# Performance work log

Hardware: AMD Instinct MI355X
Metric: run time of the kernel (lower is better)

Reference implementation:

```python
import jax, jax.numpy as jnp
import numpy as np

B, S, D, HW = 256, 32, 512, 196


def setup_inputs() -> dict:
    key = jax.random.key(0)
    ks = jax.random.split(key, 34)
    n = lambda k, sh, s=1.0: jax.random.normal(k, sh, dtype=jnp.float32) * s
    w = 0.03  # xavier-ish scale for D=512 layers
    return {
        "words": n(ks[0], (B, S, D)),
        "question": n(ks[1], (B, 2 * D)),
        "know": n(ks[2], (B, D, HW)),
        "control0": n(ks[3], (B, D)),
        "memory0": n(ks[4], (B, D)),
        # ControlUnit
        "Wsc": n(ks[5], (2 * D, D), w), "bsc": jnp.zeros((D,), jnp.float32),
        "Wp": n(ks[6], (D, D), w), "bp": jnp.zeros((D,), jnp.float32),
        "Wcq": n(ks[7], (2 * D, D), w), "bcq": jnp.zeros((D,), jnp.float32),
        "wac": n(ks[8], (D, 1), w), "bac": jnp.zeros((1,), jnp.float32),
        # ReadUnit
        "Wm": n(ks[9], (D, D), w), "bm": jnp.zeros((D,), jnp.float32),
        "Wk": n(ks[10], (D, D), w), "bk": jnp.zeros((D,), jnp.float32),
        "Wc1": n(ks[11], (3 * D, D), w), "bc1": jnp.zeros((D,), jnp.float32),
        "Wc2": n(ks[12], (D, D), w), "bc2": jnp.zeros((D,), jnp.float32),
        "war": n(ks[13], (D, 1), w), "bar": jnp.zeros((1,), jnp.float32),
        # WriteUnit (self-attention variant)
        "Wwc": n(ks[14], (D, D), w), "bwc": jnp.zeros((D,), jnp.float32),
        "waw": n(ks[15], (D, 1), w), "baw": jnp.zeros((1,), jnp.float32),
        "Wwcat": n(ks[16], (3 * D, D), w), "bwcat": jnp.zeros((D,), jnp.float32),
    }


def reference(words, question, know, control0, memory0,
              Wsc, bsc, Wp, bp, Wcq, bcq, wac, bac,
              Wm, bm, Wk, bk, Wc1, bc1, Wc2, bc2, war, bar,
              Wwc, bwc, waw, baw, Wwcat, bwcat):
    # ---- ControlUnit (step 0) ----
    q = jnp.tanh(question @ Wsc + bsc)                    # [B,D]
    pa = q @ Wp + bp                                      # position_aware[0]
    cq = jnp.concatenate([control0, pa], axis=1) @ Wcq + bcq  # [B,D]
    logit_c = (cq[:, None, :] * words) @ wac + bac        # [B,S,1]
    attn_c = jax.nn.softmax(logit_c, axis=1)
    control = jnp.sum(attn_c * words, axis=1)             # [B,D]

    # ---- ReadUnit ----
    pm = memory0 @ Wm + bm                                # [B,D]
    pk = jnp.einsum('bdn,de->ben', know, Wk) + bk[None, :, None]  # [B,D,HW]
    pm_b = jnp.broadcast_to(pm[:, :, None], pk.shape)
    feat = jnp.concatenate([pm_b * pk, pk, pm_b], axis=1)  # [B,3D,HW]
    h = jax.nn.relu(jnp.einsum('bfn,fd->bnd', feat, Wc1) + bc1)  # [B,HW,D]
    h = h @ Wc2 + bc2                                     # [B,HW,D]
    logit_r = (h * control[:, None, :]) @ war + bar       # [B,HW,1]
    a_r = jax.nn.softmax(logit_r[..., 0], axis=1)          # [B,HW]
    read = jnp.einsum('bdn,bn->bd', know, a_r)            # [B,D]

    # ---- WriteUnit (self-attention over previous controls; T=1 at step 0) ----
    sc = control @ Wwc + bwc                              # [B,D]
    ctrl_prev = control0[:, :, None]                      # [B,D,T]
    logit_w = jnp.einsum('bdt,d->bt', sc[:, :, None] * ctrl_prev, waw[:, 0]) + baw  # [B,T]
    a_w = jax.nn.softmax(logit_w, axis=1)
    attn_mem = jnp.einsum('bdt,bt->bd', memory0[:, :, None], a_w)  # [B,D]
    concat = jnp.concatenate([read, memory0, attn_mem], axis=1)    # [B,3D]
    next_mem = concat @ Wwcat + bwcat                     # [B,D]

    return control, next_mem
```

## Files before the change

### kernel.cpp

```cpp
#include <hip/hip_runtime.h>
#include <hip/hip_bf16.h>
#include <math.h>

typedef __hip_bfloat16 bf16;
typedef __attribute__((ext_vector_type(8))) short s8v;
typedef __attribute__((ext_vector_type(4))) short s4v;
typedef __attribute__((ext_vector_type(4))) float f4v;

#define BB 256
#define SS 32
#define DD 512
#define HWN 196
#define APW 72

__device__ __forceinline__ float b2f(bf16 x){ return __bfloat162float(x); }
__device__ __forceinline__ bf16 f2b(float x){ return __float2bfloat16(x); }
__device__ __forceinline__ float us2f(unsigned short u){
    union { unsigned int i; float f; } t; t.i = ((unsigned int)u) << 16; return t.f;
}
__device__ __forceinline__ float ldin(int dt, const void* p, size_t i){
    return dt ? b2f(((const bf16*)p)[i]) : ((const float*)p)[i];
}

__global__ void detect_k(const void* q, int* flag){
    __shared__ int cnt;
    if (threadIdx.x == 0) cnt = 0;
    __syncthreads();
    const unsigned short* u = (const unsigned short*)q;
    unsigned short v = u[threadIdx.x * 4];
    int e = (v >> 7) & 0xFF;
    atomicAdd(&cnt, (e >= 100 && e <= 140) ? 1 : 0);
    __syncthreads();
    if (threadIdx.x == 0) *flag = (cnt > 128) ? 1 : 0;
}

struct PJob { const void* s; const void* s_b; const void* s2; const void* s2_b;
              bf16* d; int R, C, ldd, kofs, mode, boff; };
struct PrepP { PJob j[11]; const void* war; const void* bk; float* warf; float* bkf; };

__global__ __launch_bounds__(256) void prep_k(PrepP P, const int* __restrict__ flag){
    const int dt = *flag;
    __shared__ float T[32][33];
    int bx = blockIdx.x;
    int ji = 0;
    #pragma unroll
    for (int i = 0; i < 11; ++i) if (bx >= P.j[i].boff) ji = i;
    PJob jb = P.j[ji];
    const void* src  = dt ? jb.s_b  : jb.s;
    const void* src2 = dt ? jb.s2_b : jb.s2;
    int t = bx - jb.boff;
    int tx = threadIdx.x & 31, ty = threadIdx.x >> 5;
    if (jb.mode == 3){
        for (int i = threadIdx.x; i < DD; i += 256){
            P.warf[i] = ldin(dt, P.war, i);
            P.bkf[i]  = ldin(dt, P.bk, i);
        }
        return;
    }
    int nrt = jb.R >> 5;
    int r0 = (t % nrt) << 5, c0 = (t / nrt) << 5;
    if (jb.mode == 2){
        for (int rr = ty; rr < 32; rr += 8)
            jb.d[(size_t)(r0 + rr) * jb.ldd + jb.kofs + c0 + tx] =
                f2b(ldin(dt, src, (size_t)(r0 + rr) * jb.C + c0 + tx));
        return;
    }
    for (int rr = ty; rr < 32; rr += 8){
        float v = ldin(dt, src, (size_t)(r0 + rr) * jb.C + c0 + tx);
        if (jb.mode == 1) v += ldin(dt, src2, (size_t)(r0 + rr) * jb.C + c0 + tx);
        T[rr][tx] = v;
    }
    __syncthreads();
    for (int rr = ty; rr < 32; rr += 8)
        jb.d[(size_t)(c0 + rr) * jb.ldd + jb.kofs + r0 + tx] = f2b(T[tx][rr]);
}

__global__ __launch_bounds__(256) void g1_mfma(const void* __restrict__ know,
                                               const bf16* __restrict__ BT,
                                               const float* __restrict__ bkf,
                                               bf16* __restrict__ C,
                                               int b0, int swz,
                                               const int* __restrict__ flag){
    const int dt = *flag;
    __shared__ __align__(16) bf16 As[128 * APW];
    __shared__ __align__(16) bf16 Bs[128 * APW];
    const int tid = threadIdx.x, lane = tid & 63, wave = tid >> 6;
    const int q = lane >> 4, mr = lane & 15;
    int idb = blockIdx.x, rt, ct;
    if (swz){ int g = idb >> 5, w = idb & 31; rt = g * 8 + (w & 7); ct = w >> 3; }
    else    { rt = idb >> 2; ct = idb & 3; }
    const int r0 = rt * 128, c0 = ct * 128;
    const int quad = tid >> 3;
    const int kg   = tid & 7;
    const int m    = r0 + quad * 4;
    const int bl   = m / HWN;
    const int n    = m - bl * HWN;
    const size_t abase = ((size_t)(b0 + bl) * DD) * HWN + n;
    f4v acc[2][8];
    #pragma unroll
    for (int t = 0; t < 2; ++t)
        #pragma unroll
        for (int j = 0; j < 8; ++j){ f4v z = {0.f,0.f,0.f,0.f}; acc[t][j] = z; }
    for (int k0 = 0; k0 < DD; k0 += 64){
        #pragma unroll
        for (int h = 0; h < 2; ++h){
            int kb = k0 + h * 32 + kg * 4;
            union { bf16 hh[4]; s4v v; } pk_[4];
            if (dt == 0){
                const float* kp = (const float*)know + abase + (size_t)kb * HWN;
                float4 ra  = *(const float4*)kp;
                float4 rb  = *(const float4*)(kp + HWN);
                float4 rc  = *(const float4*)(kp + 2 * HWN);
                float4 rd4 = *(const float4*)(kp + 3 * HWN);
                #pragma unroll
                for (int j = 0; j < 4; ++j){
                    pk_[j].hh[0] = f2b((&ra.x)[j]);
                    pk_[j].hh[1] = f2b((&rb.x)[j]);
                    pk_[j].hh[2] = f2b((&rc.x)[j]);
                    pk_[j].hh[3] = f2b((&rd4.x)[j]);
                }
            } else {
                const unsigned short* kp = (const unsigned short*)know + abase + (size_t)kb * HWN;
                ushort4 ua = *(const ushort4*)kp;
                ushort4 ub = *(const ushort4*)(kp + HWN);
                ushort4 uc = *(const ushort4*)(kp + 2 * HWN);
                ushort4 ud = *(const ushort4*)(kp + 3 * HWN);
                #pragma unroll
                for (int j = 0; j < 4; ++j){
                    ((unsigned short*)&pk_[j].v)[0] = (&ua.x)[j];
                    ((unsigned short*)&pk_[j].v)[1] = (&ub.x)[j];
                    ((unsigned short*)&pk_[j].v)[2] = (&uc.x)[j];
                    ((unsigned short*)&pk_[j].v)[3] = (&ud.x)[j];
                }
            }
            #pragma unroll
            for (int j = 0; j < 4; ++j)
                *(s4v*)&As[(quad * 4 + j) * APW + h * 32 + kg * 4] = pk_[j].v;
        }
        {
            int col = tid >> 1, kb = (tid & 1) * 32;
            const bf16* wp = BT + (size_t)(c0 + col) * DD + k0 + kb;
            bf16* dst = &Bs[col * APW + kb];
            #pragma unroll
            for (int t4 = 0; t4 < 32; t4 += 8)
                *(float4*)(dst + t4) = *(const float4*)(wp + t4);
        }
        __syncthreads();
        #pragma unroll
        for (int h = 0; h < 2; ++h){
            s8v a0 = *(const s8v*)&As[(wave * 32 + mr) * APW + h * 32 + q * 8];
            s8v a1 = *(const s8v*)&As[(wave * 32 + 16 + mr) * APW + h * 32 + q * 8];
            #pragma unroll
            for (int j = 0; j < 8; ++j){
                s8v b = *(const s8v*)&Bs[(j * 16 + mr) * APW + h * 32 + q * 8];
                acc[0][j] = __builtin_amdgcn_mfma_f32_16x16x32_bf16(a0, b, acc[0][j], 0, 0, 0);
                acc[1][j] = __builtin_amdgcn_mfma_f32_16x16x32_bf16(a1, b, acc[1][j], 0, 0, 0);
            }
        }
        __syncthreads();
    }
    #pragma unroll
    for (int t = 0; t < 2; ++t)
        #pragma unroll
        for (int j = 0; j < 8; ++j){
            float bb = bkf[c0 + j * 16 + mr];
            #pragma unroll
            for (int i = 0; i < 4; ++i){
                int row = r0 + wave * 32 + t * 16 + q * 4 + i;
                int col = c0 + j * 16 + mr;
                C[(size_t)row * DD + col] = f2b(acc[t][j][i] + bb);
            }
        }
}

__global__ __launch_bounds__(256) void g2_mfma(const bf16* __restrict__ Apk,
                                               const bf16* __restrict__ BT,
                                               const float* __restrict__ pmf,
                                               const float* __restrict__ t3b,
                                               const float* __restrict__ uf,
                                               float* __restrict__ lpart,
                                               int b0, int swz){
    __shared__ __align__(16) bf16 As[128 * APW];
    __shared__ __align__(16) bf16 Bs[128 * APW];
    const int tid = threadIdx.x, lane = tid & 63, wave = tid >> 6;
    const int q = lane >> 4, mr = lane & 15;
    int idb = blockIdx.x, u, ct;
    if (swz){ int g = idb >> 5, w = idb & 31; u = g * 8 + (w & 7); ct = w >> 3; }
    else    { u = idb >> 2; ct = idb & 3; }
    const int bl = u >> 1, rt = u & 1;
    const int b = b0 + bl;
    const int c0 = ct * 128, rbase = rt * 128;
    const float* pmb = pmf + (size_t)b * DD;
    f4v acc[2][8];
    #pragma unroll
    for (int t = 0; t < 2; ++t)
        #pragma unroll
        for (int j = 0; j < 8; ++j){ f4v z = {0.f,0.f,0.f,0.f}; acc[t][j] = z; }
    for (int k0 = 0; k0 < DD; k0 += 64){
        {
            int row = tid >> 1, kb = (tid & 1) * 32;
            int rl = rbase + row;
            bf16* dst = &As[row * APW + kb];
            if (rl < HWN){
                const bf16* ap = Apk + ((size_t)bl * HWN + rl) * DD + k0 + kb;
                #pragma unroll
                for (int t4 = 0; t4 < 32; t4 += 8)
                    *(float4*)(dst + t4) = *(const float4*)(ap + t4);
            } else {
                float4 z = {0.f,0.f,0.f,0.f};
                #pragma unroll
                for (int t4 = 0; t4 < 32; t4 += 8)
                    *(float4*)(dst + t4) = z;
            }
        }
        {
            int col = tid >> 1, kb = (tid & 1) * 32;
            const bf16* wrow = BT + (size_t)(c0 + col) * (2 * DD) + k0 + kb;
            bf16* dst = &Bs[col * APW + kb];
            #pragma unroll
            for (int t4 = 0; t4 < 32; t4 += 8){
                union { bf16 h[8]; float4 f; } w1, w2, be;
                w1.f = *(const float4*)(wrow + t4);
                w2.f = *(const float4*)(wrow + DD + t4);
                float4 pA = *(const float4*)(pmb + k0 + kb + t4);
                float4 pB = *(const float4*)(pmb + k0 + kb + t4 + 4);
                #pragma unroll
                for (int j = 0; j < 4; ++j){
                    be.h[j]     = f2b((&pA.x)[j] * b2f(w1.h[j])     + b2f(w2.h[j]));
                    be.h[4 + j] = f2b((&pB.x)[j] * b2f(w1.h[4 + j]) + b2f(w2.h[4 + j]));
                }
                *(float4*)(dst + t4) = be.f;
            }
        }
        __syncthreads();
        #pragma unroll
        for (int h = 0; h < 2; ++h){
            s8v a0 = *(const s8v*)&As[(wave * 32 + mr) * APW + h * 32 + q * 8];
            s8v a1 = *(const s8v*)&As[(wave * 32 + 16 + mr) * APW + h * 32 + q * 8];
            #pragma unroll
            for (int j = 0; j < 8; ++j){
                s8v b2 = *(const s8v*)&Bs[(j * 16 + mr) * APW + h * 32 + q * 8];
                acc[0][j] = __builtin_amdgcn_mfma_f32_16x16x32_bf16(a0, b2, acc[0][j], 0, 0, 0);
                acc[1][j] = __builtin_amdgcn_mfma_f32_16x16x32_bf16(a1, b2, acc[1][j], 0, 0, 0);
            }
        }
        __syncthreads();
    }
    float part[2][4] = {};
    #pragma unroll
    for (int t = 0; t < 2; ++t)
        #pragma unroll
        for (int j = 0; j < 8; ++j)
            #pragma unroll
            for (int i = 0; i < 4; ++i){
                int rl = rbase + wave * 32 + t * 16 + q * 4 + i;
                if (rl < HWN){
                    int col = c0 + j * 16 + mr;
                    float hv = acc[t][j][i] + t3b[(size_t)b * DD + col];
                    part[t][i] += fmaxf(hv, 0.f) * uf[(size_t)b * DD + col];
                }
            }
    #pragma unroll
    for (int t = 0; t < 2; ++t)
        #pragma unroll
        for (int i = 0; i < 4; ++i){
            float v = part[t][i];
            v += __shfl_xor(v, 1, 16);
            v += __shfl_xor(v, 2, 16);
            v += __shfl_xor(v, 4, 16);
            v += __shfl_xor(v, 8, 16);
            int rl = rbase + wave * 32 + t * 16 + q * 4 + i;
            if (mr == 0 && rl < HWN)
                lpart[(size_t)ct * (BB * HWN) + (size_t)b * HWN + rl] = v;
        }
}

struct SSeg { const void* A; int a_ws, lda, K, koff; };
struct SP {
    SSeg s[2]; int nseg;
    const bf16* BT; int ldb;
    const float* amul;
    const void* bias;
    float* C; int M, N, act;
    void* out2; int o2off;
};
struct SPP { SP j[2]; };

__global__ __launch_bounds__(256) void sgemm_k(SPP P, const int* __restrict__ flag){
    const int dt = *flag;
    const SP p = P.j[blockIdx.z];
    const int tid = threadIdx.x, lane = tid & 63, w = tid >> 6;
    const int q = lane >> 4, mr = lane & 15;
    const int n0 = blockIdx.x * 16, m0 = blockIdx.y * 64 + w * 16;
    f4v acc = {0.f,0.f,0.f,0.f};
    for (int sg = 0; sg < p.nseg; ++sg){
        const SSeg s = p.s[sg];
        const float* amul = (sg == 0) ? p.amul : nullptr;
        #pragma unroll 4
        for (int k0 = 0; k0 < s.K; k0 += 32){
            const int kk = k0 + q * 8;
            union { bf16 h[8]; s8v v; } a;
            if (s.a_ws || dt == 0){
                const float* Af = (const float*)s.A + (size_t)(m0 + mr) * s.lda + kk;
                float4 f0 = *(const float4*)Af;
                float4 f1 = *(const float4*)(Af + 4);
                float f[8] = {f0.x, f0.y, f0.z, f0.w, f1.x, f1.y, f1.z, f1.w};
                if (amul){
                    #pragma unroll
                    for (int j = 0; j < 8; ++j) f[j] *= amul[kk + j];
                }
                #pragma unroll
                for (int j = 0; j < 8; ++j) a.h[j] = f2b(f[j]);
            } else {
                a.v = *(const s8v*)((const bf16*)s.A + (size_t)(m0 + mr) * s.lda + kk);
                if (amul){
                    #pragma unroll
                    for (int j = 0; j < 8; ++j) a.h[j] = f2b(b2f(a.h[j]) * amul[kk + j]);
                }
            }
            s8v b = *(const s8v*)(p.BT + (size_t)(n0 + mr) * p.ldb + s.koff + kk);
            acc = __builtin_amdgcn_mfma_f32_16x16x32_bf16(a.v, b, acc, 0, 0, 0);
        }
    }
    #pragma unroll
    for (int i = 0; i < 4; ++i){
        int row = m0 + q * 4 + i, col = n0 + mr;
        float v = acc[i] + (p.bias ? ldin(dt, p.bias, col) : 0.f);
        if (p.act == 1) v = tanhf(v);
        p.C[(size_t)row * p.N + col] = v;
        if (p.out2){
            size_t oi = (size_t)p.o2off + (size_t)row * p.N + col;
            if (dt) ((bf16*)p.out2)[oi] = f2b(v);
            else    ((float*)p.out2)[oi] = v;
        }
    }
}

__global__ __launch_bounds__(256) void attn_control_k(const float* __restrict__ cq,
                                                      const void* __restrict__ wac,
                                                      const void* __restrict__ bac,
                                                      const void* __restrict__ words,
                                                      float* __restrict__ control,
                                                      const void* __restrict__ bc2,
                                                      const float* __restrict__ warf,
                                                      const void* __restrict__ bar,
                                                      float* __restrict__ bias_r,
                                                      void* __restrict__ out,
                                                      const int* __restrict__ flag){
    const int dt = *flag;
    const int b = blockIdx.x, tid = threadIdx.x;
    __shared__ float cw[DD];
    __shared__ float lg[SS];
    __shared__ float es[SS];
    __shared__ float red[256];
    for (int d = tid; d < DD; d += 256) cw[d] = cq[(size_t)b*DD + d] * ldin(dt, wac, d);
    __syncthreads();
    int s = tid >> 3, l8 = tid & 7;
    float p = 0.f;
    for (int d = l8; d < DD; d += 8) p += cw[d] * ldin(dt, words, ((size_t)b*SS + s)*DD + d);
    for (int off = 4; off; off >>= 1) p += __shfl_down(p, off, 8);
    if (l8 == 0) lg[s] = p + ldin(dt, bac, 0);
    __syncthreads();
    if (tid == 0){
        float mx = -INFINITY;
        for (int i = 0; i < SS; ++i) mx = fmaxf(mx, lg[i]);
        float sm = 0.f;
        for (int i = 0; i < SS; ++i){ es[i] = expf(lg[i] - mx); sm += es[i]; }
        float inv = 1.f / sm;
        for (int i = 0; i < SS; ++i) es[i] *= inv;
    }
    __syncthreads();
    float vb = 0.f;
    for (int d = tid; d < DD; d += 256){
        float c = 0.f;
        #pragma unroll 8
        for (int s2 = 0; s2 < SS; ++s2) c += es[s2] * ldin(dt, words, ((size_t)b*SS + s2)*DD + d);
        control[(size_t)b*DD + d] = c;
        if (dt) ((bf16*)out)[(size_t)b*DD + d] = f2b(c);
        else    ((float*)out)[(size_t)b*DD + d] = c;
        vb += ldin(dt, bc2, d) * c * warf[d];
    }
    red[tid] = vb; __syncthreads();
    for (int off = 128; off; off >>= 1){ if (tid < off) red[tid] += red[tid + off]; __syncthreads(); }
    if (tid == 0) bias_r[b] = red[0] + ldin(dt, bar, 0);
}

__global__ __launch_bounds__(256) void softmax_read_k(const float* __restrict__ lpart,
                                                      const float* __restrict__ bias_r,
                                                      const void* __restrict__ know,
                                                      float* __restrict__ readout,
                                                      const int* __restrict__ flag){
    const int dt = *flag;
    const int b = blockIdx.x, tid = threadIdx.x;
    __shared__ float a[HWN];
    __shared__ float red[256];
    float x = -INFINITY;
    if (tid < HWN){
        float sacc = bias_r[b];
        #pragma unroll
        for (int c = 0; c < 4; ++c)
            sacc += lpart[(size_t)c * (BB * HWN) + (size_t)b * HWN + tid];
        x = sacc;
    }
    red[tid] = x; __syncthreads();
    for (int off = 128; off; off >>= 1){ if (tid < off) red[tid] = fmaxf(red[tid], red[tid + off]); __syncthreads(); }
    float mx = red[0]; __syncthreads();
    float e = (tid < HWN) ? expf(x - mx) : 0.f;
    red[tid] = e; __syncthreads();
    for (int off = 128; off; off >>= 1){ if (tid < off) red[tid] += red[tid + off]; __syncthreads(); }
    float inv = 1.f / red[0];
    if (tid < HWN) a[tid] = e * inv;
    __syncthreads();
    for (int d = tid; d < DD; d += 256){
        size_t base = ((size_t)b*DD + d) * HWN;
        float sum = 0.f;
        if (dt){
            const ushort4* k4 = (const ushort4*)((const unsigned short*)know + base);
            #pragma unroll 7
            for (int c = 0; c < HWN/4; ++c){
                ushort4 u4 = k4[c];
                sum += a[4*c+0]*us2f(u4.x) + a[4*c+1]*us2f(u4.y)
                     + a[4*c+2]*us2f(u4.z) + a[4*c+3]*us2f(u4.w);
            }
        } else {
            const float4* k4 = (const float4*)((const float*)know + base);
            #pragma unroll 7
            for (int c = 0; c < HWN/4; ++c){
                float4 f4 = k4[c];
                sum += a[4*c+0]*f4.x + a[4*c+1]*f4.y + a[4*c+2]*f4.z + a[4*c+3]*f4.w;
            }
        }
        readout[(size_t)b*DD + d] = sum;
    }
}

extern "C" void kernel_launch(void* const* d_in, const int* in_sizes, int n_in,
                              void* d_out, int out_size, void* d_ws, size_t ws_size,
                              hipStream_t stream){
    const void* words    = d_in[0];
    const void* question = d_in[1];
    const void* know     = d_in[2];
    const void* control0 = d_in[3];
    const void* memory0  = d_in[4];
    const void* Wsc = d_in[5];   const void* bsc = d_in[6];
    const void* Wp  = d_in[7];   const void* bp  = d_in[8];
    const void* Wcq = d_in[9];   const void* bcq = d_in[10];
    const void* wac = d_in[11];  const void* bac = d_in[12];
    const void* Wm  = d_in[13];  const void* bm  = d_in[14];
    const void* Wk  = d_in[15];  const void* bk  = d_in[16];
    const void* Wc1 = d_in[17];  const void* bc1 = d_in[18];
    const void* Wc2 = d_in[19];  const void* bc2 = d_in[20];
    const void* war = d_in[21];  const void* bar = d_in[22];
    const void* Wwcat = d_in[27]; const void* bwcat = d_in[28];

    int* flag = (int*)d_ws;
    float* F = ((float*)d_ws) + 16;
    const int NBD = BB * DD;
    float* q_   = F;
    float* pa   = F + 1*NBD;
    float* cq   = F + 2*NBD;
    float* ctrl = F + 3*NBD;
    float* pm   = F + 4*NBD;
    float* t3b  = F + 5*NBD;
    float* u_   = F + 6*NBD;
    float* rd   = F + 7*NBD;
    float* nm   = F + 8*NBD;
    float* bias_r = F + 9*NBD;
    float* warf   = bias_r + BB;
    float* bkf    = warf + DD;
    float* lpart  = bkf + DD;
    size_t off_f = 16 + 9*(size_t)NBD + BB + 2*DD + 8*(size_t)BB*HWN;
    size_t byte_off = (off_f * 4 + 255) & ~(size_t)255;
    bf16* WB = (bf16*)((char*)d_ws + byte_off);
    bf16* WscT   = WB;
    bf16* WcqT   = WscT  + (size_t)DD*2*DD;
    bf16* Wc1T2  = WcqT  + (size_t)DD*2*DD;
    bf16* WwcatF = Wc1T2 + (size_t)DD*2*DD;
    bf16* WpT    = WwcatF+ (size_t)DD*2*DD;
    bf16* WmT    = WpT   + (size_t)DD*DD;
    bf16* Wc1t3T = WmT   + (size_t)DD*DD;
    bf16* WkT    = Wc1t3T+ (size_t)DD*DD;
    bf16* Wc2cv  = WkT   + (size_t)DD*DD;
    size_t big_off = (byte_off + ((size_t)DD*2*DD*4 + (size_t)DD*DD*5) * sizeof(bf16) + 255) & ~(size_t)255;

    size_t per_batch = (size_t)HWN * DD * sizeof(bf16);
    size_t avail = (ws_size > big_off) ? (ws_size - big_off) : 0;
    int CB = (int)(avail / per_batch);
    CB &= ~31;
    if (CB > BB) CB = BB;
    if (CB < 32) CB = 32;
    bf16* pkT = (bf16*)((char*)d_ws + big_off);

    dim3 blk(256);

    detect_k<<<dim3(1), blk, 0, stream>>>(question, flag);

    {
        PrepP P; int bo = 0;
        auto J = [&](const void* s, const void* sb, const void* s2, const void* s2b,
                     bf16* d, int R, int C, int ldd, int kofs, int mode, int idx){
            int nb = (mode == 3) ? 1 : ((R >> 5) * (C >> 5));
            P.j[idx] = PJob{ s, sb, s2, s2b, d, R, C, ldd, kofs, mode, bo };
            bo += nb;
        };
        const void* Wc1t3_f = (const void*)((const float*)Wc1 + (size_t)2*DD*DD);
        const void* Wc1t3_b = (const void*)((const bf16*) Wc1 + (size_t)2*DD*DD);
        const void* Ww1_f = (const void*)((const float*)Wwcat + (size_t)DD*DD);
        const void* Ww1_b = (const void*)((const bf16*) Wwcat + (size_t)DD*DD);
        const void* Ww2_f = (const void*)((const float*)Wwcat + (size_t)2*DD*DD);
        const void* Ww2_b = (const void*)((const bf16*) Wwcat + (size_t)2*DD*DD);
        J(Wsc,   Wsc,   nullptr, nullptr, WscT,   2*DD, DD, 2*DD, 0,   0, 0);
        J(Wp,    Wp,    nullptr, nullptr, WpT,    DD,   DD, DD,   0,   0, 1);
        J(Wcq,   Wcq,   nullptr, nullptr, WcqT,   2*DD, DD, 2*DD, 0,   0, 2);
        J(Wm,    Wm,    nullptr, nullptr, WmT,    DD,   DD, DD,   0,   0, 3);
        J(Wc1,   Wc1,   nullptr, nullptr, Wc1T2,  2*DD, DD, 2*DD, 0,   0, 4);
        J(Wc1t3_f, Wc1t3_b, nullptr, nullptr, Wc1t3T, DD, DD, DD, 0,   0, 5);
        J(Wk,    Wk,    nullptr, nullptr, WkT,    DD,   DD, DD,   0,   0, 6);
        J(Wwcat, Wwcat, nullptr, nullptr, WwcatF, DD,   DD, 2*DD, 0,   0, 7);
        J(Ww1_f, Ww1_b, Ww2_f,   Ww2_b,   WwcatF, DD,   DD, 2*DD, 512, 1, 8);
        J(Wc2,   Wc2,   nullptr, nullptr, Wc2cv,  DD,   DD, DD,   0,   2, 9);
        J(nullptr,nullptr,nullptr,nullptr,nullptr,0,    0,  0,    0,   3, 10);
        P.war = war; P.bk = bk; P.warf = warf; P.bkf = bkf;
        prep_k<<<dim3(bo), blk, 0, stream>>>(P, flag);
    }

    SPP P2;
    auto mkjob = [&](SP& p){ p = SP{}; };

    mkjob(P2.j[0]);
    P2.j[0].nseg = 1;
    P2.j[0].s[0] = SSeg{ question, 0, 2*DD, 2*DD, 0 };
    P2.j[0].BT = WscT; P2.j[0].ldb = 2*DD;
    P2.j[0].bias = bsc; P2.j[0].C = q_; P2.j[0].M = BB; P2.j[0].N = DD; P2.j[0].act = 1;
    mkjob(P2.j[1]);
    P2.j[1].nseg = 1;
    P2.j[1].s[0] = SSeg{ memory0, 0, DD, DD, 0 };
    P2.j[1].BT = WmT; P2.j[1].ldb = DD;
    P2.j[1].bias = bm; P2.j[1].C = pm; P2.j[1].M = BB; P2.j[1].N = DD; P2.j[1].act = 0;
    sgemm_k<<<dim3(DD/16, BB/64, 2), blk, 0, stream>>>(P2, flag);

    mkjob(P2.j[0]);
    P2.j[0].nseg = 1;
    P2.j[0].s[0] = SSeg{ q_, 1, DD, DD, 0 };
    P2.j[0].BT = WpT; P2.j[0].ldb = DD;
    P2.j[0].bias = bp; P2.j[0].C = pa; P2.j[0].M = BB; P2.j[0].N = DD; P2.j[0].act = 0;
    mkjob(P2.j[1]);
    P2.j[1].nseg = 1;
    P2.j[1].s[0] = SSeg{ pm, 1, DD, DD, 0 };
    P2.j[1].BT = Wc1t3T; P2.j[1].ldb = DD;
    P2.j[1].bias = bc1; P2.j[1].C = t3b; P2.j[1].M = BB; P2.j[1].N = DD; P2.j[1].act = 0;
    sgemm_k<<<dim3(DD/16, BB/64, 2), blk, 0, stream>>>(P2, flag);

    mkjob(P2.j[0]);
    P2.j[0].nseg = 2;
    P2.j[0].s[0] = SSeg{ control0, 0, DD, DD, 0 };
    P2.j[0].s[1] = SSeg{ pa,       1, DD, DD, 512 };
    P2.j[0].BT = WcqT; P2.j[0].ldb = 2*DD;
    P2.j[0].bias = bcq; P2.j[0].C = cq; P2.j[0].M = BB; P2.j[0].N = DD; P2.j[0].act = 0;
    sgemm_k<<<dim3(DD/16, BB/64, 1), blk, 0, stream>>>(P2, flag);

    attn_control_k<<<dim3(BB), blk, 0, stream>>>(cq, wac, bac, words, ctrl,
                                                 bc2, warf, bar, bias_r, d_out, flag);

    mkjob(P2.j[0]);
    P2.j[0].nseg = 1;
    P2.j[0].s[0] = SSeg{ ctrl, 1, DD, DD, 0 };
    P2.j[0].BT = Wc2cv; P2.j[0].ldb = DD; P2.j[0].amul = warf;
    P2.j[0].C = u_; P2.j[0].M = BB; P2.j[0].N = DD; P2.j[0].act = 0;
    sgemm_k<<<dim3(DD/16, BB/64, 1), blk, 0, stream>>>(P2, flag);

    for (int b0 = 0; b0 < BB; b0 += CB){
        int cb = (b0 + CB <= BB) ? CB : (BB - b0);
        int M = cb * HWN;
        int nR = M / 128;
        int swz1 = (nR % 8 == 0) ? 1 : 0;
        g1_mfma<<<dim3(4 * nR), blk, 0, stream>>>(know, WkT, bkf, pkT, b0, swz1, flag);
        int nU = cb * 2;
        int swz2 = (nU % 8 == 0) ? 1 : 0;
        g2_mfma<<<dim3(4 * nU), blk, 0, stream>>>(pkT, Wc1T2, pm, t3b, u_, lpart, b0, swz2);
    }

    softmax_read_k<<<dim3(BB), blk, 0, stream>>>(lpart, bias_r, know, rd, flag);

    mkjob(P2.j[0]);
    P2.j[0].nseg = 2;
    P2.j[0].s[0] = SSeg{ rd,      1, DD, DD, 0 };
    P2.j[0].s[1] = SSeg{ memory0, 0, DD, DD, 512 };
    P2.j[0].BT = WwcatF; P2.j[0].ldb = 2*DD;
    P2.j[0].bias = bwcat; P2.j[0].C = nm; P2.j[0].M = BB; P2.j[0].N = DD; P2.j[0].act = 0;
    P2.j[0].out2 = d_out; P2.j[0].o2off = NBD;
    sgemm_k<<<dim3(DD/16, BB/64, 1), blk, 0, stream>>>(P2, flag);
}
```

Baseline: 556.8 us.

## Double-buffer GEMMs with swizzled LDS and async loads; move pm multiply into g1

Both MFMA GEMM kernels now double-buffer their LDS tiles. B (and A in g2) are staged with global_load_lds direct-to-LDS copies into an XOR-swizzled layout, which replaces the padded layout as the way to avoid bank conflicts. g1 now writes a [rows,1024] operand holding pm*pk and pk, so g2 becomes a plain K=1024 GEMM over flattened rows and no longer mixes pm into the weights per batch inside its B staging. The cost is doubled intermediate storage and write traffic, and g2 rows now span batch boundaries instead of being padded per batch.

```diff
diff --git a/kernel.cpp b/kernel.cpp
--- a/kernel.cpp
+++ b/kernel.cpp
@@ -11,7 +11,6 @@
 #define SS 32
 #define DD 512
 #define HWN 196
-#define APW 72
 
 __device__ __forceinline__ float b2f(bf16 x){ return __bfloat162float(x); }
 __device__ __forceinline__ bf16 f2b(float x){ return __float2bfloat16(x); }
@@ -20,6 +19,11 @@
 }
 __device__ __forceinline__ float ldin(int dt, const void* p, size_t i){
     return dt ? b2f(((const bf16*)p)[i]) : ((const float*)p)[i];
+}
+__device__ __forceinline__ void g2l16(void* lds, const void* gsrc){
+    __builtin_amdgcn_global_load_lds(
+        (const __attribute__((address_space(1))) unsigned int*)gsrc,
+        (__attribute__((address_space(3))) unsigned int*)lds, 16, 0, 0);
 }
 
 __global__ void detect_k(const void* q, int* flag){
@@ -75,15 +79,20 @@
         jb.d[(size_t)(c0 + rr) * jb.ldd + jb.kofs + r0 + tx] = f2b(T[tx][rr]);
 }
 
+__device__ __forceinline__ int swzo(int row, int slot){
+    return row * 128 + ((slot ^ (row & 7)) << 4);
+}
+
 __global__ __launch_bounds__(256) void g1_mfma(const void* __restrict__ know,
                                                const bf16* __restrict__ BT,
                                                const float* __restrict__ bkf,
-                                               bf16* __restrict__ C,
+                                               const float* __restrict__ pmf,
+                                               bf16* __restrict__ A2,
                                                int b0, int swz,
                                                const int* __restrict__ flag){
     const int dt = *flag;
-    __shared__ __align__(16) bf16 As[128 * APW];
-    __shared__ __align__(16) bf16 Bs[128 * APW];
+    __shared__ __align__(16) char lA[2][128 * 128];
+    __shared__ __align__(16) char lB[2][128 * 128];
     const int tid = threadIdx.x, lane = tid & 63, wave = tid >> 6;
     const int q = lane >> 4, mr = lane & 15;
     int idb = blockIdx.x, rt, ct;
@@ -96,182 +105,213 @@
     const int bl   = m / HWN;
     const int n    = m - bl * HWN;
     const size_t abase = ((size_t)(b0 + bl) * DD) * HWN + n;
+
+    float4  fr[2][4];
+    ushort4 ur[2][4];
     f4v acc[2][8];
     #pragma unroll
     for (int t = 0; t < 2; ++t)
         #pragma unroll
         for (int j = 0; j < 8; ++j){ f4v z = {0.f,0.f,0.f,0.f}; acc[t][j] = z; }
-    for (int k0 = 0; k0 < DD; k0 += 64){
+
+    auto issueA = [&](int t){
         #pragma unroll
         for (int h = 0; h < 2; ++h){
-            int kb = k0 + h * 32 + kg * 4;
-            union { bf16 hh[4]; s4v v; } pk_[4];
+            const int kb = t * 64 + h * 32 + kg * 4;
             if (dt == 0){
                 const float* kp = (const float*)know + abase + (size_t)kb * HWN;
-                float4 ra  = *(const float4*)kp;
-                float4 rb  = *(const float4*)(kp + HWN);
-                float4 rc  = *(const float4*)(kp + 2 * HWN);
-                float4 rd4 = *(const float4*)(kp + 3 * HWN);
+                fr[h][0] = *(const float4*)kp;
+                fr[h][1] = *(const float4*)(kp + HWN);
+                fr[h][2] = *(const float4*)(kp + 2 * HWN);
+                fr[h][3] = *(const float4*)(kp + 3 * HWN);
+            } else {
+                const unsigned short* kp = (const unsigned short*)know + abase + (size_t)kb * HWN;
+                ur[h][0] = *(const ushort4*)kp;
+                ur[h][1] = *(const ushort4*)(kp + HWN);
+                ur[h][2] = *(const ushort4*)(kp + 2 * HWN);
+                ur[h][3] = *(const ushort4*)(kp + 3 * HWN);
+            }
+        }
+    };
+    auto writeA = [&](int buf){
+        #pragma unroll
+        for (int h = 0; h < 2; ++h){
+            union { bf16 hh[4]; unsigned short uu[4]; s4v v; } col[4];
+            if (dt == 0){
                 #pragma unroll
                 for (int j = 0; j < 4; ++j){
-                    pk_[j].hh[0] = f2b((&ra.x)[j]);
-                    pk_[j].hh[1] = f2b((&rb.x)[j]);
-                    pk_[j].hh[2] = f2b((&rc.x)[j]);
-                    pk_[j].hh[3] = f2b((&rd4.x)[j]);
+                    col[j].hh[0] = f2b((&fr[h][0].x)[j]);
+                    col[j].hh[1] = f2b((&fr[h][1].x)[j]);
+                    col[j].hh[2] = f2b((&fr[h][2].x)[j]);
+                    col[j].hh[3] = f2b((&fr[h][3].x)[j]);
                 }
             } else {
-                const unsigned short* kp = (const unsigned short*)know + abase + (size_t)kb * HWN;
-                ushort4 ua = *(const ushort4*)kp;
-                ushort4 ub = *(const ushort4*)(kp + HWN);
-                ushort4 uc = *(const ushort4*)(kp + 2 * HWN);
-                ushort4 ud = *(const ushort4*)(kp + 3 * HWN);
                 #pragma unroll
                 for (int j = 0; j < 4; ++j){
-                    ((unsigned short*)&pk_[j].v)[0] = (&ua.x)[j];
-                    ((unsigned short*)&pk_[j].v)[1] = (&ub.x)[j];
-                    ((unsigned short*)&pk_[j].v)[2] = (&uc.x)[j];
-                    ((unsigned short*)&pk_[j].v)[3] = (&ud.x)[j];
+                    col[j].uu[0] = (&ur[h][0].x)[j];
+                    col[j].uu[1] = (&ur[h][1].x)[j];
+                    col[j].uu[2] = (&ur[h][2].x)[j];
+                    col[j].uu[3] = (&ur[h][3].x)[j];
                 }
             }
+            const int slot = h * 4 + (kg >> 1);
+            const int sub  = (kg & 1) << 3;
             #pragma unroll
-            for (int j = 0; j < 4; ++j)
-                *(s4v*)&As[(quad * 4 + j) * APW + h * 32 + kg * 4] = pk_[j].v;
-        }
-        {
-            int col = tid >> 1, kb = (tid & 1) * 32;
-            const bf16* wp = BT + (size_t)(c0 + col) * DD + k0 + kb;
-            bf16* dst = &Bs[col * APW + kb];
-            #pragma unroll
-            for (int t4 = 0; t4 < 32; t4 += 8)
-                *(float4*)(dst + t4) = *(const float4*)(wp + t4);
-        }
-        __syncthreads();
+            for (int j = 0; j < 4; ++j){
+                const int row = quad * 4 + j;
+                *(s4v*)&lA[buf][row * 128 + (((slot ^ (row & 7))) << 4) + sub] = col[j].v;
+            }
+        }
+    };
+    auto stageB = [&](int t, int buf){
+        #pragma unroll
+        for (int c = 0; c < 4; ++c){
+            const int r0c = (c * 4 + wave) * 8;
+            const int row = r0c + (lane >> 3);
+            const int ls  = (lane & 7) ^ (row & 7);
+            g2l16(&lB[buf][r0c * 128], BT + (size_t)(c0 + row) * DD + t * 64 + ls * 8);
+        }
+    };
+    auto mfmaStep = [&](int buf){
         #pragma unroll
         for (int h = 0; h < 2; ++h){
-            s8v a0 = *(const s8v*)&As[(wave * 32 + mr) * APW + h * 32 + q * 8];
-            s8v a1 = *(const s8v*)&As[(wave * 32 + 16 + mr) * APW + h * 32 + q * 8];
+            const int slot = h * 4 + q;
+            const int ra0 = wave * 32 + mr, ra1 = ra0 + 16;
+            s8v a0 = *(const s8v*)&lA[buf][swzo(ra0, slot)];
+            s8v a1 = *(const s8v*)&lA[buf][swzo(ra1, slot)];
             #pragma unroll
             for (int j = 0; j < 8; ++j){
-                s8v b = *(const s8v*)&Bs[(j * 16 + mr) * APW + h * 32 + q * 8];
-                acc[0][j] = __builtin_amdgcn_mfma_f32_16x16x32_bf16(a0, b, acc[0][j], 0, 0, 0);
-                acc[1][j] = __builtin_amdgcn_mfma_f32_16x16x32_bf16(a1, b, acc[1][j], 0, 0, 0);
-            }
-        }
+                const int rb = j * 16 + mr;
+                s8v bb = *(const s8v*)&lB[buf][swzo(rb, slot)];
+                acc[0][j] = __builtin_amdgcn_mfma_f32_16x16x32_bf16(a0, bb, acc[0][j], 0, 0, 0);
+                acc[1][j] = __builtin_amdgcn_mfma_f32_16x16x32_bf16(a1, bb, acc[1][j], 0, 0, 0);
+            }
+        }
+    };
+
+    issueA(0); stageB(0, 0);
+    writeA(0);
+    __syncthreads();
+    int cur = 0;
+    for (int t = 0; t < 8; ++t){
+        if (t < 7){ stageB(t + 1, cur ^ 1); issueA(t + 1); }
+        mfmaStep(cur);
+        if (t < 7) writeA(cur ^ 1);
         __syncthreads();
-    }
+        cur ^= 1;
+    }
+
     #pragma unroll
-    for (int t = 0; t < 2; ++t)
+    for (int tt = 0; tt < 2; ++tt)
         #pragma unroll
         for (int j = 0; j < 8; ++j){
-            float bb = bkf[c0 + j * 16 + mr];
+            const int col = c0 + j * 16 + mr;
+            const float bv = bkf[col];
             #pragma unroll
             for (int i = 0; i < 4; ++i){
-                int row = r0 + wave * 32 + t * 16 + q * 4 + i;
-                int col = c0 + j * 16 + mr;
-                C[(size_t)row * DD + col] = f2b(acc[t][j][i] + bb);
-            }
-        }
-}
-
-__global__ __launch_bounds__(256) void g2_mfma(const bf16* __restrict__ Apk,
+                const int row = r0 + wave * 32 + tt * 16 + q * 4 + i;
+                const int blr = row / HWN;
+                const float v = acc[tt][j][i] + bv;
+                const float pmv = pmf[(size_t)(b0 + blr) * DD + col];
+                A2[(size_t)row * 1024 + col]       = f2b(v * pmv);
+                A2[(size_t)row * 1024 + 512 + col] = f2b(v);
+            }
+        }
+}
+
+__global__ __launch_bounds__(256) void g2_mfma(const bf16* __restrict__ A2,
                                                const bf16* __restrict__ BT,
-                                               const float* __restrict__ pmf,
                                                const float* __restrict__ t3b,
                                                const float* __restrict__ uf,
                                                float* __restrict__ lpart,
                                                int b0, int swz){
-    __shared__ __align__(16) bf16 As[128 * APW];
-    __shared__ __align__(16) bf16 Bs[128 * APW];
+    __shared__ __align__(16) char lA[2][128 * 128];
+    __shared__ __align__(16) char lB[2][128 * 128];
     const int tid = threadIdx.x, lane = tid & 63, wave = tid >> 6;
     const int q = lane >> 4, mr = lane & 15;
-    int idb = blockIdx.x, u, ct;
-    if (swz){ int g = idb >> 5, w = idb & 31; u = g * 8 + (w & 7); ct = w >> 3; }
-    else    { u = idb >> 2; ct = idb & 3; }
-    const int bl = u >> 1, rt = u & 1;
-    const int b = b0 + bl;
-    const int c0 = ct * 128, rbase = rt * 128;
-    const float* pmb = pmf + (size_t)b * DD;
+    int idb = blockIdx.x, rt, ct;
+    if (swz){ int g = idb >> 5, w = idb & 31; rt = g * 8 + (w & 7); ct = w >> 3; }
+    else    { rt = idb >> 2; ct = idb & 3; }
+    const int r0 = rt * 128, c0 = ct * 128;
     f4v acc[2][8];
     #pragma unroll
     for (int t = 0; t < 2; ++t)
         #pragma unroll
         for (int j = 0; j < 8; ++j){ f4v z = {0.f,0.f,0.f,0.f}; acc[t][j] = z; }
-    for (int k0 = 0; k0 < DD; k0 += 64){
-        {
-            int row = tid >> 1, kb = (tid & 1) * 32;
-            int rl = rbase + row;
-            bf16* dst = &As[row * APW + kb];
-            if (rl < HWN){
-                const bf16* ap = Apk + ((size_t)bl * HWN + rl) * DD + k0 + kb;
-                #pragma unroll
-                for (int t4 = 0; t4 < 32; t4 += 8)
-                    *(float4*)(dst + t4) = *(const float4*)(ap + t4);
-            } else {
-                float4 z = {0.f,0.f,0.f,0.f};
-                #pragma unroll
-                for (int t4 = 0; t4 < 32; t4 += 8)
-                    *(float4*)(dst + t4) = z;
-            }
-        }
-        {
-            int col = tid >> 1, kb = (tid & 1) * 32;
-            const bf16* wrow = BT + (size_t)(c0 + col) * (2 * DD) + k0 + kb;
-            bf16* dst = &Bs[col * APW + kb];
-            #pragma unroll
-            for (int t4 = 0; t4 < 32; t4 += 8){
-                union { bf16 h[8]; float4 f; } w1, w2, be;
-                w1.f = *(const float4*)(wrow + t4);
-                w2.f = *(const float4*)(wrow + DD + t4);
-                float4 pA = *(const float4*)(pmb + k0 + kb + t4);
-                float4 pB = *(const float4*)(pmb + k0 + kb + t4 + 4);
-                #pragma unroll
-                for (int j = 0; j < 4; ++j){
-                    be.h[j]     = f2b((&pA.x)[j] * b2f(w1.h[j])     + b2f(w2.h[j]));
-                    be.h[4 + j] = f2b((&pB.x)[j] * b2f(w1.h[4 + j]) + b2f(w2.h[4 + j]));
-                }
-                *(float4*)(dst + t4) = be.f;
-            }
-        }
-        __syncthreads();
+
+    auto stageA = [&](int t, int buf){
+        #pragma unroll
+        for (int c = 0; c < 4; ++c){
+            const int r0c = (c * 4 + wave) * 8;
+            const int row = r0c + (lane >> 3);
+            const int ls  = (lane & 7) ^ (row & 7);
+            g2l16(&lA[buf][r0c * 128], A2 + (size_t)(r0 + row) * 1024 + t * 64 + ls * 8);
+        }
+    };
+    auto stageB = [&](int t, int buf){
+        #pragma unroll
+        for (int c = 0; c < 4; ++c){
+            const int r0c = (c * 4 + wave) * 8;
+            const int row = r0c + (lane >> 3);
+            const int ls  = (lane & 7) ^ (row & 7);
+            g2l16(&lB[buf][r0c * 128], BT + (size_t)(c0 + row) * 1024 + t * 64 + ls * 8);
+        }
+    };
+    auto mfmaStep = [&](int buf){
         #pragma unroll
         for (int h = 0; h < 2; ++h){
-            s8v a0 = *(const s8v*)&As[(wave * 32 + mr) * APW + h * 32 + q * 8];
-            s8v a1 = *(const s8v*)&As[(wave * 32 + 16 + mr) * APW + h * 32 + q * 8];
+            const int slot = h * 4 + q;
+            const int ra0 = wave * 32 + mr, ra1 = ra0 + 16;
+            s8v a0 = *(const s8v*)&lA[buf][swzo(ra0, slot)];
+            s8v a1 = *(const s8v*)&lA[buf][swzo(ra1, slot)];
             #pragma unroll
             for (int j = 0; j < 8; ++j){
-                s8v b2 = *(const s8v*)&Bs[(j * 16 + mr) * APW + h * 32 + q * 8];
-                acc[0][j] = __builtin_amdgcn_mfma_f32_16x16x32_bf16(a0, b2, acc[0][j], 0, 0, 0);
-                acc[1][j] = __builtin_amdgcn_mfma_f32_16x16x32_bf16(a1, b2, acc[1][j], 0, 0, 0);
-            }
-        }
+                const int rb = j * 16 + mr;
+                s8v bb = *(const s8v*)&lB[buf][swzo(rb, slot)];
+                acc[0][j] = __builtin_amdgcn_mfma_f32_16x16x32_bf16(a0, bb, acc[0][j], 0, 0, 0);
+                acc[1][j] = __builtin_amdgcn_mfma_f32_16x16x32_bf16(a1, bb, acc[1][j], 0, 0, 0);
+            }
+        }
+    };
+
+    stageA(0, 0); stageB(0, 0);
+    __syncthreads();
+    int cur = 0;
+    for (int t = 0; t < 16; ++t){
+        if (t < 15){ stageA(t + 1, cur ^ 1); stageB(t + 1, cur ^ 1); }
+        mfmaStep(cur);
         __syncthreads();
-    }
-    float part[2][4] = {};
+        cur ^= 1;
+    }
+
+    float part[2][4] = {{0.f,0.f,0.f,0.f},{0.f,0.f,0.f,0.f}};
     #pragma unroll
-    for (int t = 0; t < 2; ++t)
-        #pragma unroll
-        for (int j = 0; j < 8; ++j)
+    for (int tt = 0; tt < 2; ++tt)
+        #pragma unroll
+        for (int j = 0; j < 8; ++j){
+            const int col = c0 + j * 16 + mr;
             #pragma unroll
             for (int i = 0; i < 4; ++i){
-                int rl = rbase + wave * 32 + t * 16 + q * 4 + i;
-                if (rl < HWN){
-                    int col = c0 + j * 16 + mr;
-                    float hv = acc[t][j][i] + t3b[(size_t)b * DD + col];
-                    part[t][i] += fmaxf(hv, 0.f) * uf[(size_t)b * DD + col];
-                }
-            }
+                const int row = r0 + wave * 32 + tt * 16 + q * 4 + i;
+                const int blr = row / HWN;
+                const int b = b0 + blr;
+                const float hv = acc[tt][j][i] + t3b[(size_t)b * DD + col];
+                part[tt][i] += fmaxf(hv, 0.f) * uf[(size_t)b * DD + col];
+            }
+        }
     #pragma unroll
-    for (int t = 0; t < 2; ++t)
+    for (int tt = 0; tt < 2; ++tt)
         #pragma unroll
         for (int i = 0; i < 4; ++i){
-            float v = part[t][i];
+            float v = part[tt][i];
             v += __shfl_xor(v, 1, 16);
             v += __shfl_xor(v, 2, 16);
             v += __shfl_xor(v, 4, 16);
             v += __shfl_xor(v, 8, 16);
-            int rl = rbase + wave * 32 + t * 16 + q * 4 + i;
-            if (mr == 0 && rl < HWN)
-                lpart[(size_t)ct * (BB * HWN) + (size_t)b * HWN + rl] = v;
+            const int row = r0 + wave * 32 + tt * 16 + q * 4 + i;
+            const int blr = row / HWN, rl = row - blr * HWN;
+            if (mr == 0)
+                lpart[(size_t)ct * (BB * HWN) + (size_t)(b0 + blr) * HWN + rl] = v;
         }
 }
 
@@ -483,13 +523,13 @@
     bf16* Wc2cv  = WkT   + (size_t)DD*DD;
     size_t big_off = (byte_off + ((size_t)DD*2*DD*4 + (size_t)DD*DD*5) * sizeof(bf16) + 255) & ~(size_t)255;
 
-    size_t per_batch = (size_t)HWN * DD * sizeof(bf16);
+    size_t per_batch = (size_t)HWN * 1024 * sizeof(bf16);
     size_t avail = (ws_size > big_off) ? (ws_size - big_off) : 0;
     int CB = (int)(avail / per_batch);
     CB &= ~31;
     if (CB > BB) CB = BB;
     if (CB < 32) CB = 32;
-    bf16* pkT = (bf16*)((char*)d_ws + big_off);
+    bf16* A2 = (bf16*)((char*)d_ws + big_off);
 
     dim3 blk(256);
 
@@ -571,13 +611,10 @@
 
     for (int b0 = 0; b0 < BB; b0 += CB){
         int cb = (b0 + CB <= BB) ? CB : (BB - b0);
-        int M = cb * HWN;
-        int nR = M / 128;
-        int swz1 = (nR % 8 == 0) ? 1 : 0;
-        g1_mfma<<<dim3(4 * nR), blk, 0, stream>>>(know, WkT, bkf, pkT, b0, swz1, flag);
-        int nU = cb * 2;
-        int swz2 = (nU % 8 == 0) ? 1 : 0;
-        g2_mfma<<<dim3(4 * nU), blk, 0, stream>>>(pkT, Wc1T2, pm, t3b, u_, lpart, b0, swz2);
+        int nR = cb * 49 / 32;
+        int swzf = (nR % 8 == 0) ? 1 : 0;
+        g1_mfma<<<dim3(nR * 4), blk, 0, stream>>>(know, WkT, bkf, pm, A2, b0, swzf, flag);
+        g2_mfma<<<dim3(nR * 4), blk, 0, stream>>>(A2, Wc1T2, t3b, u_, lpart, b0, swzf);
     }
 
     softmax_read_k<<<dim3(BB), blk, 0, stream>>>(lpart, bias_r, know, rd, flag);
```

Result: slower. 607.4 us (+9.1%).
